# Kernel optimization log

Measured on AMD Instinct MI355X. Metric: run time of the kernel, lower is better.

Reference implementation:

```python
import jax, jax.numpy as jnp
import numpy as np

D_MODEL = 1024
N_HEADS = 16
D_K = D_MODEL // N_HEADS  # 64
SCALE = 1.0 / np.sqrt(D_K).astype(np.float32)


def setup_inputs() -> dict:
    key = jax.random.key(0)
    kx, kq, kk, kv, ko = jax.random.split(key, 5)
    B, S = 2, 2048
    s = 0.02  # keep pre-softmax logits in a sane range
    return {
        "x": jax.random.normal(kx, (B, S, D_MODEL), dtype=jnp.float32),
        "Wq": jax.random.normal(kq, (D_MODEL, D_MODEL), dtype=jnp.float32) * s,
        "Wk": jax.random.normal(kk, (D_MODEL, D_MODEL), dtype=jnp.float32) * s,
        "Wv": jax.random.normal(kv, (D_MODEL, D_MODEL), dtype=jnp.float32) * s,
        "Wo": jax.random.normal(ko, (D_MODEL, D_MODEL), dtype=jnp.float32) * s,
    }


def reference(x, Wq, Wk, Wv, Wo):
    # x: [B, S, D]; nn.Linear(bias=False) computes x @ W.T
    B, S, D = x.shape
    H, dk = N_HEADS, D_K

    def proj(W):
        # [B, S, D] -> [B, H, S, dk]
        return (x @ W.T).reshape(B, S, H, dk).transpose(0, 2, 1, 3)

    q = proj(Wq)
    k = proj(Wk)
    v = proj(Wv)

    # Flash tiling with online softmax is exact full attention (no mask):
    scores = jnp.einsum("bhqd,bhkd->bhqk", q, k) * SCALE  # [B,H,S,S]
    p = jax.nn.softmax(scores, axis=-1)
    o = jnp.einsum("bhqk,bhkd->bhqd", p, v)               # [B,H,S,dk]

    o = o.transpose(0, 2, 1, 3).reshape(B, S, D)
    return o @ Wo.T
```

## Files before the change

### kernel.cpp

```cpp
#include <hip/hip_runtime.h>
#include <cstdint>

typedef __attribute__((ext_vector_type(8))) __bf16 bf16x8;
typedef __attribute__((ext_vector_type(4))) float f32x4;
using u16 = unsigned short;
using u32 = unsigned int;

#define D_MODEL 1024
#define N_HEADS 16
#define D_K     64
#define SEQ     2048
#define BATCH   2
#define NTOKENS (BATCH * SEQ)
#define SCALE   0.125f
#define LOG2E   1.44269504088896340736f
#define C2      (SCALE * LOG2E)

__device__ __forceinline__ u16 f32_to_bf16(float f) {
    union { float f; u32 u; } v; v.f = f;
    u32 r = (v.u + 0x7fffu + ((v.u >> 16) & 1u)) >> 16;
    return (u16)r;
}

__device__ __forceinline__ u32 cvt_pk_bf16(float a, float b) {
    u32 r;
    asm("v_cvt_pk_bf16_f32 %0, %1, %2" : "=v"(r) : "v"(a), "v"(b));
    return r;
}

typedef const __attribute__((address_space(1))) u32* gas_ptr;
typedef __attribute__((address_space(3))) u32* las_ptr;
__device__ __forceinline__ void gl2lds16(const u16* g, u16* l) {
    __builtin_amdgcn_global_load_lds((gas_ptr)g, (las_ptr)l, 16, 0, 0);
}

__global__ __launch_bounds__(256) void cvt_all(const float* __restrict__ x,
                                               const float* __restrict__ Wq, const float* __restrict__ Wk,
                                               const float* __restrict__ Wv, const float* __restrict__ Wo,
                                               u16* __restrict__ xb,
                                               u16* __restrict__ wq, u16* __restrict__ wk,
                                               u16* __restrict__ wv, u16* __restrict__ wo) {
    const int NX = NTOKENS * D_MODEL;
    size_t i = (size_t)(blockIdx.x * 256 + threadIdx.x) * 4;
    const float* src; u16* dst; size_t off;
    if (i < (size_t)NX) { src = x; dst = xb; off = i; }
    else {
        size_t j = i - NX;
        int w = (int)(j >> 20);
        off = j & ((1u << 20) - 1);
        src = (w == 0) ? Wq : (w == 1) ? Wk : (w == 2) ? Wv : Wo;
        dst = (w == 0) ? wq : (w == 1) ? wk : (w == 2) ? wv : wo;
    }
    float4 f = *(const float4*)(src + off);
    u32 lo = (u32)f32_to_bf16(f.x) | ((u32)f32_to_bf16(f.y) << 16);
    u32 hi = (u32)f32_to_bf16(f.z) | ((u32)f32_to_bf16(f.w) << 16);
    uint2 o; o.x = lo; o.y = hi;
    *(uint2*)(dst + off) = o;
}

__global__ __launch_bounds__(256) void gemm_qkv(const u16* __restrict__ xb,
                                                const u16* __restrict__ wq,
                                                const u16* __restrict__ wk,
                                                const u16* __restrict__ wv,
                                                u16* __restrict__ Qb, u16* __restrict__ Kb,
                                                u16* __restrict__ Vt) {
    __shared__ __align__(16) u16 As[2][128 * 32];
    __shared__ __align__(16) u16 Bs[2][128 * 32];

    const int tid  = threadIdx.x;
    const int wave = tid >> 6, lane = tid & 63;
    const int quad = lane >> 4, l4 = lane & 15;
    const int wm = wave >> 1, wn = wave & 1;
    const int f = blockIdx.x;

    const u16 *Abase, *Bbase;
    if (f < 512) {
        const int m0 = (f & 31) * 128, t = f >> 5;
        Abase = xb + (size_t)m0 * D_MODEL;
        Bbase = ((t < 8) ? wq : wk) + (size_t)(t & 7) * 128 * D_MODEL;
    } else {
        const int g = f - 512;
        Abase = wv + (size_t)(g & 7) * 128 * D_MODEL;
        Bbase = xb + (size_t)(g >> 3) * 128 * D_MODEL;
    }

    f32x4 acc[4][4] = {};

    const int r0 = wave * 16 + (lane >> 2);
    const int ch = (lane & 3) * 8;
    const u16* Ag0 = Abase + (size_t)r0 * D_MODEL + ch;
    const u16* Bg0 = Bbase + (size_t)r0 * D_MODEL + ch;
    u16* AsW0 = As[0] + wave * 512;
    u16* AsW1 = As[1] + wave * 512;
    u16* BsW0 = Bs[0] + wave * 512;
    u16* BsW1 = Bs[1] + wave * 512;

    for (int kt = 0; kt < 16; ++kt) {
        const int ko = kt * 64;
        __syncthreads();
        gl2lds16(Ag0 + ko, AsW0);
        gl2lds16(Ag0 + (size_t)64 * D_MODEL + ko, AsW0 + 2048);
        gl2lds16(Bg0 + ko, BsW0);
        gl2lds16(Bg0 + (size_t)64 * D_MODEL + ko, BsW0 + 2048);
        gl2lds16(Ag0 + ko + 32, AsW1);
        gl2lds16(Ag0 + (size_t)64 * D_MODEL + ko + 32, AsW1 + 2048);
        gl2lds16(Bg0 + ko + 32, BsW1);
        gl2lds16(Bg0 + (size_t)64 * D_MODEL + ko + 32, BsW1 + 2048);
        __syncthreads();

#pragma unroll
        for (int s = 0; s < 2; ++s) {
            bf16x8 af[4], bfr[4];
#pragma unroll
            for (int mt = 0; mt < 4; mt++)
                af[mt] = *(const bf16x8*)&As[s][(wm * 64 + mt * 16 + l4) * 32 + quad * 8];
#pragma unroll
            for (int nt = 0; nt < 4; nt++)
                bfr[nt] = *(const bf16x8*)&Bs[s][(wn * 64 + nt * 16 + l4) * 32 + quad * 8];
#pragma unroll
            for (int mt = 0; mt < 4; mt++)
#pragma unroll
                for (int nt = 0; nt < 4; nt++)
                    acc[mt][nt] = __builtin_amdgcn_mfma_f32_16x16x32_bf16(af[mt], bfr[nt], acc[mt][nt], 0, 0, 0);
        }
    }

#pragma unroll
    for (int mt = 0; mt < 4; mt++)
#pragma unroll
        for (int nt = 0; nt < 4; nt++)
#pragma unroll
            for (int r = 0; r < 4; r++) {
                int mrow = wm * 64 + mt * 16 + quad * 4 + r;
                int ncol = wn * 64 + nt * 16 + l4;
                float v = acc[mt][nt][r];
                if (f < 512) {
                    const int m0 = (f & 31) * 128, t = f >> 5;
                    if (t < 8)
                        Qb[(size_t)(m0 + mrow) * D_MODEL + (t & 7) * 128 + ncol] = f32_to_bf16(v * C2);
                    else
                        Kb[(size_t)(m0 + mrow) * D_MODEL + (t & 7) * 128 + ncol] = f32_to_bf16(v);
                } else {
                    const int g = f - 512;
                    Vt[(size_t)((g & 7) * 128 + mrow) * NTOKENS + (g >> 3) * 128 + ncol] = f32_to_bf16(v);
                }
            }
}

__global__ __launch_bounds__(256) void gemm_out(const u16* __restrict__ A,
                                                const u16* __restrict__ Bw,
                                                float* __restrict__ C) {
    __shared__ __align__(16) u16 As[2][128 * 32];
    __shared__ __align__(16) u16 Bs[2][128 * 32];

    const int tid  = threadIdx.x;
    const int wave = tid >> 6, lane = tid & 63;
    const int quad = lane >> 4, l4 = lane & 15;
    const int wm = wave >> 1, wn = wave & 1;
    const int m0 = (blockIdx.x & 31) * 128, n0 = (blockIdx.x >> 5) * 128;

    f32x4 acc[4][4] = {};

    const int r0 = wave * 16 + (lane >> 2);
    const int ch = (lane & 3) * 8;
    const u16* Ag0 = A  + (size_t)(m0 + r0) * D_MODEL + ch;
    const u16* Bg0 = Bw + (size_t)(n0 + r0) * D_MODEL + ch;
    u16* AsW0 = As[0] + wave * 512;
    u16* AsW1 = As[1] + wave * 512;
    u16* BsW0 = Bs[0] + wave * 512;
    u16* BsW1 = Bs[1] + wave * 512;

    for (int kt = 0; kt < 16; ++kt) {
        const int ko = kt * 64;
        __syncthreads();
        gl2lds16(Ag0 + ko, AsW0);
        gl2lds16(Ag0 + (size_t)64 * D_MODEL + ko, AsW0 + 2048);
        gl2lds16(Bg0 + ko, BsW0);
        gl2lds16(Bg0 + (size_t)64 * D_MODEL + ko, BsW0 + 2048);
        gl2lds16(Ag0 + ko + 32, AsW1);
        gl2lds16(Ag0 + (size_t)64 * D_MODEL + ko + 32, AsW1 + 2048);
        gl2lds16(Bg0 + ko + 32, BsW1);
        gl2lds16(Bg0 + (size_t)64 * D_MODEL + ko + 32, BsW1 + 2048);
        __syncthreads();

#pragma unroll
        for (int s = 0; s < 2; ++s) {
            bf16x8 af[4], bfr[4];
#pragma unroll
            for (int mt = 0; mt < 4; mt++)
                af[mt] = *(const bf16x8*)&As[s][(wm * 64 + mt * 16 + l4) * 32 + quad * 8];
#pragma unroll
            for (int nt = 0; nt < 4; nt++)
                bfr[nt] = *(const bf16x8*)&Bs[s][(wn * 64 + nt * 16 + l4) * 32 + quad * 8];
#pragma unroll
            for (int mt = 0; mt < 4; mt++)
#pragma unroll
                for (int nt = 0; nt < 4; nt++)
                    acc[mt][nt] = __builtin_amdgcn_mfma_f32_16x16x32_bf16(af[mt], bfr[nt], acc[mt][nt], 0, 0, 0);
        }
    }

#pragma unroll
    for (int mt = 0; mt < 4; mt++)
#pragma unroll
        for (int nt = 0; nt < 4; nt++)
#pragma unroll
            for (int r = 0; r < 4; r++) {
                int mrow = wm * 64 + mt * 16 + quad * 4 + r;
                int ncol = wn * 64 + nt * 16 + l4;
                C[(size_t)(m0 + mrow) * D_MODEL + n0 + ncol] = acc[mt][nt][r];
            }
}

__global__ __launch_bounds__(512, 4) void attn(const u16* __restrict__ Q,
                                               const u16* __restrict__ K,
                                               const u16* __restrict__ Vt,
                                               u16* __restrict__ O) {
    __shared__ __align__(16) u16 smem[17664];
    u16* KsB = smem;
    u16* VsB = smem + 8192;
    const int KBUF = 4096, VBUF = 4096;

    const int tid  = threadIdx.x;
    const int wave = tid >> 6, lane = tid & 63;
    const int quad = lane >> 4, l4 = lane & 15;
    const int qg = wave & 3, kv = wave >> 2;
    const int bid = blockIdx.x;
    const int h  = (bid & 7) | (((bid >> 3) & 1) << 3);
    const int b  = (bid >> 4) & 1;
    const int q0 = (bid >> 5) * 128;
    const size_t headoff = (size_t)b * SEQ * D_MODEL + (size_t)h * D_K;

    const int sarr = tid >> 8;
    const int st   = tid & 255;
    const int srow = st >> 2, sc = st & 3;
    const int r7   = srow & 7;
    const u16* gsrc = (sarr == 0)
        ? K  + headoff + (size_t)srow * D_MODEL + sc * 16
        : Vt + (size_t)(h * 64 + srow) * NTOKENS + (size_t)b * SEQ + sc * 16;
    const size_t gstep = (sarr == 0) ? (size_t)64 * D_MODEL : 64;

    const int kd0 = srow * 64 + (((2 * sc)     ^ r7) * 8);
    const int kd1 = srow * 64 + (((2 * sc + 1) ^ r7) * 8);
    const int g32 = sc >> 1, vc = sc & 1;
    const int vw0 = srow * 64 + (((g32 * 4 + 0) ^ r7) * 8) + 4 * vc;
    const int vw1 = srow * 64 + (((g32 * 4 + 1) ^ r7) * 8) + 4 * vc;
    const int vw2 = srow * 64 + (((g32 * 4 + 2) ^ r7) * 8) + 4 * vc;
    const int vw3 = srow * 64 + (((g32 * 4 + 3) ^ r7) * 8) + 4 * vc;

    bf16x8 qa[2][2];
#pragma unroll
    for (int qs = 0; qs < 2; qs++) {
        const u16* qp = Q + headoff + (size_t)(q0 + qg * 32 + qs * 16 + l4) * D_MODEL + quad * 8;
        qa[qs][0] = *(const bf16x8*)qp;
        qa[qs][1] = *(const bf16x8*)(qp + 32);
    }

    union { u32 u[4]; bf16x8 v; } onesu;
#pragma unroll
    for (int i = 0; i < 4; i++) onesu.u[i] = 0x3F803F80u;

    int4 pr0 = *(const int4*)gsrc;
    int4 pr1 = *(const int4*)(gsrc + 8);

    f32x4 acc_o[2][4] = {};
    f32x4 acc_l[2] = {};

    const int sw7 = l4 & 7;

    for (int it = 0; it < 32; ++it) {
        if (sarr == 0) {
            u16* d = KsB + (it & 1) * KBUF;
            *(int4*)(d + kd0) = pr0;
            *(int4*)(d + kd1) = pr1;
        } else {
            u16* d = VsB + (it & 1) * VBUF;
            const uint2* h0 = (const uint2*)&pr0;
            const uint2* h1 = (const uint2*)&pr1;
            *(uint2*)(d + vw0) = h0[0];
            *(uint2*)(d + vw1) = h0[1];
            *(uint2*)(d + vw2) = h1[0];
            *(uint2*)(d + vw3) = h1[1];
        }
        __syncthreads();

        const u16* gn = gsrc + (size_t)((it + 1) & 31) * gstep;
        pr0 = *(const int4*)gn;
        pr1 = *(const int4*)(gn + 8);

        const u16* ksr = KsB + (it & 1) * KBUF;
        const u16* vsr = VsB + (it & 1) * VBUF;

        bf16x8 kb[2][2];
#pragma unroll
        for (int n2 = 0; n2 < 2; n2++) {
            const int krow = kv * 32 + n2 * 16 + l4;
            kb[n2][0] = *(const bf16x8*)&ksr[krow * 64 + ((quad       ^ sw7) * 8)];
            kb[n2][1] = *(const bf16x8*)&ksr[krow * 64 + (((4 + quad) ^ sw7) * 8)];
        }
        f32x4 sacc[2][2] = {};
        __builtin_amdgcn_s_setprio(1);
#pragma unroll
        for (int qs = 0; qs < 2; qs++)
#pragma unroll
            for (int n2 = 0; n2 < 2; n2++) {
                sacc[qs][n2] = __builtin_amdgcn_mfma_f32_16x16x32_bf16(kb[n2][0], qa[qs][0], sacc[qs][n2], 0, 0, 0);
                sacc[qs][n2] = __builtin_amdgcn_mfma_f32_16x16x32_bf16(kb[n2][1], qa[qs][1], sacc[qs][n2], 0, 0, 0);
            }
        __builtin_amdgcn_s_setprio(0);

        union { u32 u[4]; bf16x8 v; } pp[2];
#pragma unroll
        for (int qs = 0; qs < 2; qs++)
#pragma unroll
            for (int n2 = 0; n2 < 2; n2++) {
                float p0 = __builtin_amdgcn_exp2f(sacc[qs][n2][0]);
                float p1 = __builtin_amdgcn_exp2f(sacc[qs][n2][1]);
                float p2 = __builtin_amdgcn_exp2f(sacc[qs][n2][2]);
                float p3 = __builtin_amdgcn_exp2f(sacc[qs][n2][3]);
                pp[qs].u[n2 * 2]     = cvt_pk_bf16(p0, p1);
                pp[qs].u[n2 * 2 + 1] = cvt_pk_bf16(p2, p3);
            }

        __builtin_amdgcn_s_setprio(1);
#pragma unroll
        for (int dvt = 0; dvt < 4; dvt++) {
            const int vrow = dvt * 16 + l4;
            bf16x8 vfr = *(const bf16x8*)&vsr[vrow * 64 + ((((kv << 2) + quad) ^ sw7) * 8)];
#pragma unroll
            for (int qs = 0; qs < 2; qs++)
                acc_o[qs][dvt] = __builtin_amdgcn_mfma_f32_16x16x32_bf16(pp[qs].v, vfr, acc_o[qs][dvt], 0, 0, 0);
        }
#pragma unroll
        for (int qs = 0; qs < 2; qs++)
            acc_l[qs] = __builtin_amdgcn_mfma_f32_16x16x32_bf16(pp[qs].v, onesu.v, acc_l[qs], 0, 0, 0);
        __builtin_amdgcn_s_setprio(0);
    }

    const int OFS = 68;
    float* Of = (float*)smem;
    float* Lf = Of + 128 * OFS;
    __syncthreads();
    if (kv == 1) {
#pragma unroll
        for (int qs = 0; qs < 2; qs++) {
#pragma unroll
            for (int dvt = 0; dvt < 4; dvt++)
#pragma unroll
                for (int r = 0; r < 4; r++)
                    Of[(qg * 32 + qs * 16 + quad * 4 + r) * OFS + dvt * 16 + l4] = acc_o[qs][dvt][r];
            if (l4 == 0)
#pragma unroll
                for (int r = 0; r < 4; r++)
                    Lf[qg * 32 + qs * 16 + quad * 4 + r] = acc_l[qs][r];
        }
    }
    __syncthreads();
    if (kv == 0) {
#pragma unroll
        for (int qs = 0; qs < 2; qs++)
#pragma unroll
            for (int r = 0; r < 4; r++) {
                const int qi = qg * 32 + qs * 16 + quad * 4 + r;
                float ltot = acc_l[qs][r] + Lf[qi];
                float linv = 1.f / ltot;
                const int qrow = q0 + qi;
#pragma unroll
                for (int dvt = 0; dvt < 4; dvt++) {
                    float v = acc_o[qs][dvt][r] + Of[qi * OFS + dvt * 16 + l4];
                    O[headoff + (size_t)qrow * D_MODEL + dvt * 16 + l4] = f32_to_bf16(v * linv);
                }
            }
    }
}

extern "C" void kernel_launch(void* const* d_in, const int* in_sizes, int n_in,
                              void* d_out, int out_size, void* d_ws, size_t ws_size,
                              hipStream_t stream) {
    const float* x  = (const float*)d_in[0];
    const float* Wq = (const float*)d_in[1];
    const float* Wk = (const float*)d_in[2];
    const float* Wv = (const float*)d_in[3];
    const float* Wo = (const float*)d_in[4];

    const int NW = D_MODEL * D_MODEL;

    char* ws = (char*)d_ws;
    u16* xb = (u16*)ws;
    u16* wq = (u16*)(ws + (8u << 20));
    u16* wk = wq + NW;
    u16* wv = wk + NW;
    u16* wo = wv + NW;
    u16* Qb  = (u16*)(ws + (16u << 20));
    u16* Kb  = (u16*)(ws + (24u << 20));
    u16* Vtb = (u16*)(ws + (32u << 20));

    cvt_all<<<8192, 256, 0, stream>>>(x, Wq, Wk, Wv, Wo, xb, wq, wk, wv, wo);

    gemm_qkv<<<768, 256, 0, stream>>>(xb, wq, wk, wv, Qb, Kb, Vtb);

    attn<<<512, 512, 0, stream>>>(Qb, Kb, Vtb, xb);

    gemm_out<<<256, 256, 0, stream>>>(xb, wo, (float*)d_out);
}
```

Before: 183.4 us.

## Restructure GEMM core with prefetch pipelining and pre-swizzled global layout

```diff
diff --git a/kernel.cpp b/kernel.cpp
--- a/kernel.cpp
+++ b/kernel.cpp
@@ -55,159 +55,143 @@
     u32 lo = (u32)f32_to_bf16(f.x) | ((u32)f32_to_bf16(f.y) << 16);
     u32 hi = (u32)f32_to_bf16(f.z) | ((u32)f32_to_bf16(f.w) << 16);
     uint2 o; o.x = lo; o.y = hi;
-    *(uint2*)(dst + off) = o;
-}
-
-__global__ __launch_bounds__(256) void gemm_qkv(const u16* __restrict__ xb,
-                                                const u16* __restrict__ wq,
-                                                const u16* __restrict__ wk,
-                                                const u16* __restrict__ wv,
-                                                u16* __restrict__ Qb, u16* __restrict__ Kb,
-                                                u16* __restrict__ Vt) {
-    __shared__ __align__(16) u16 As[2][128 * 32];
-    __shared__ __align__(16) u16 Bs[2][128 * 32];
-
+    size_t osw = (off & ~(size_t)63) | ((((off >> 3) & 7) ^ ((off >> 10) & 7)) << 3) | (off & 7);
+    *(uint2*)(dst + osw) = o;
+}
+
+__device__ __forceinline__ void gemm_core_128(const u16* __restrict__ Ab,
+                                              const u16* __restrict__ Bb,
+                                              u16* __restrict__ sm,
+                                              f32x4 acc[4][4]) {
     const int tid  = threadIdx.x;
     const int wave = tid >> 6, lane = tid & 63;
-    const int quad = lane >> 4, l4 = lane & 15;
+    const int quad = lane >> 4, l4 = lane & 15, s7 = l4 & 7;
     const int wm = wave >> 1, wn = wave & 1;
-    const int f = blockIdx.x;
-
-    const u16 *Abase, *Bbase;
-    if (f < 512) {
-        const int m0 = (f & 31) * 128, t = f >> 5;
-        Abase = xb + (size_t)m0 * D_MODEL;
-        Bbase = ((t < 8) ? wq : wk) + (size_t)(t & 7) * 128 * D_MODEL;
+
+    const int srow = tid >> 3, sch = tid & 7;
+    const u16* Asrc = Ab + (size_t)srow * D_MODEL + sch * 8;
+    const u16* Bsrc = Bb + (size_t)srow * D_MODEL + sch * 8;
+
+#define STG8(base_, kt_) do {                                                         \
+    const size_t ko_ = (size_t)(kt_) * 64;                                            \
+    u16* const Ad_ = sm + (base_) + wave * 512;                                       \
+    u16* const Bd_ = sm + (base_) + 8192 + wave * 512;                                \
+    _Pragma("unroll")                                                                 \
+    for (int c_ = 0; c_ < 4; c_++)                                                    \
+        gl2lds16(Asrc + (size_t)c_ * 32 * D_MODEL + ko_, Ad_ + c_ * 2048);            \
+    _Pragma("unroll")                                                                 \
+    for (int c_ = 0; c_ < 4; c_++)                                                    \
+        gl2lds16(Bsrc + (size_t)c_ * 32 * D_MODEL + ko_, Bd_ + c_ * 2048);            \
+} while (0)
+
+    STG8(0, 0);
+    asm volatile("s_waitcnt vmcnt(0)" ::: "memory");
+    __builtin_amdgcn_s_barrier();
+
+    for (int kt = 0; kt < 16; ++kt) {
+        const int cur = (kt & 1) << 14;
+        if (kt < 15) {
+            if (kt & 1) STG8(0, kt + 1); else STG8(16384, kt + 1);
+        }
+        const u16* Ar = sm + cur;
+        const u16* Br = sm + cur + 8192;
+        bf16x8 af[4][2], bfr[4][2];
+#pragma unroll
+        for (int mt = 0; mt < 4; mt++) {
+            const int row = wm * 64 + mt * 16 + l4;
+#pragma unroll
+            for (int kk = 0; kk < 2; kk++)
+                af[mt][kk] = *(const bf16x8*)&Ar[row * 64 + (((kk << 2) + quad) ^ s7) * 8];
+        }
+#pragma unroll
+        for (int nt = 0; nt < 4; nt++) {
+            const int row = wn * 64 + nt * 16 + l4;
+#pragma unroll
+            for (int kk = 0; kk < 2; kk++)
+                bfr[nt][kk] = *(const bf16x8*)&Br[row * 64 + (((kk << 2) + quad) ^ s7) * 8];
+        }
+        __builtin_amdgcn_s_setprio(1);
+#pragma unroll
+        for (int kk = 0; kk < 2; kk++)
+#pragma unroll
+            for (int mt = 0; mt < 4; mt++)
+#pragma unroll
+                for (int nt = 0; nt < 4; nt++)
+                    acc[mt][nt] = __builtin_amdgcn_mfma_f32_16x16x32_bf16(af[mt][kk], bfr[nt][kk], acc[mt][nt], 0, 0, 0);
+        __builtin_amdgcn_s_setprio(0);
+        asm volatile("s_waitcnt vmcnt(0)" ::: "memory");
+        __builtin_amdgcn_s_barrier();
+    }
+#undef STG8
+}
+
+__global__ __launch_bounds__(256, 2) void gemm_qkv(const u16* __restrict__ xb,
+                                                   const u16* __restrict__ wq,
+                                                   const u16* __restrict__ wk,
+                                                   const u16* __restrict__ wv,
+                                                   u16* __restrict__ Qb, u16* __restrict__ Kb,
+                                                   u16* __restrict__ Vt) {
+    __shared__ __align__(16) u16 sm[32768];
+    const int bid = blockIdx.x;
+    const u16 *Ab, *Bb;
+    int m0, n0, sel;
+    if (bid < 512) {
+        sel = bid >> 8;
+        const int t = bid & 255;
+        m0 = (t >> 3) * 128; n0 = (t & 7) * 128;
+        Ab = xb + (size_t)m0 * D_MODEL;
+        Bb = (sel ? wk : wq) + (size_t)n0 * D_MODEL;
     } else {
-        const int g = f - 512;
-        Abase = wv + (size_t)(g & 7) * 128 * D_MODEL;
-        Bbase = xb + (size_t)(g >> 3) * 128 * D_MODEL;
+        sel = 2;
+        const int t = bid - 512;
+        m0 = (t >> 5) * 128; n0 = (t & 31) * 128;
+        Ab = wv + (size_t)m0 * D_MODEL;
+        Bb = xb + (size_t)n0 * D_MODEL;
     }
 
     f32x4 acc[4][4] = {};
-
-    const int r0 = wave * 16 + (lane >> 2);
-    const int ch = (lane & 3) * 8;
-    const u16* Ag0 = Abase + (size_t)r0 * D_MODEL + ch;
-    const u16* Bg0 = Bbase + (size_t)r0 * D_MODEL + ch;
-    u16* AsW0 = As[0] + wave * 512;
-    u16* AsW1 = As[1] + wave * 512;
-    u16* BsW0 = Bs[0] + wave * 512;
-    u16* BsW1 = Bs[1] + wave * 512;
-
-    for (int kt = 0; kt < 16; ++kt) {
-        const int ko = kt * 64;
-        __syncthreads();
-        gl2lds16(Ag0 + ko, AsW0);
-        gl2lds16(Ag0 + (size_t)64 * D_MODEL + ko, AsW0 + 2048);
-        gl2lds16(Bg0 + ko, BsW0);
-        gl2lds16(Bg0 + (size_t)64 * D_MODEL + ko, BsW0 + 2048);
-        gl2lds16(Ag0 + ko + 32, AsW1);
-        gl2lds16(Ag0 + (size_t)64 * D_MODEL + ko + 32, AsW1 + 2048);
-        gl2lds16(Bg0 + ko + 32, BsW1);
-        gl2lds16(Bg0 + (size_t)64 * D_MODEL + ko + 32, BsW1 + 2048);
-        __syncthreads();
-
-#pragma unroll
-        for (int s = 0; s < 2; ++s) {
-            bf16x8 af[4], bfr[4];
-#pragma unroll
-            for (int mt = 0; mt < 4; mt++)
-                af[mt] = *(const bf16x8*)&As[s][(wm * 64 + mt * 16 + l4) * 32 + quad * 8];
-#pragma unroll
-            for (int nt = 0; nt < 4; nt++)
-                bfr[nt] = *(const bf16x8*)&Bs[s][(wn * 64 + nt * 16 + l4) * 32 + quad * 8];
-#pragma unroll
-            for (int mt = 0; mt < 4; mt++)
-#pragma unroll
-                for (int nt = 0; nt < 4; nt++)
-                    acc[mt][nt] = __builtin_amdgcn_mfma_f32_16x16x32_bf16(af[mt], bfr[nt], acc[mt][nt], 0, 0, 0);
-        }
-    }
-
+    gemm_core_128(Ab, Bb, sm, acc);
+
+    const int lane = threadIdx.x & 63, quad = lane >> 4, l4 = lane & 15;
+    const int wave = threadIdx.x >> 6, wm = wave >> 1, wn = wave & 1;
 #pragma unroll
     for (int mt = 0; mt < 4; mt++)
 #pragma unroll
         for (int nt = 0; nt < 4; nt++)
 #pragma unroll
             for (int r = 0; r < 4; r++) {
-                int mrow = wm * 64 + mt * 16 + quad * 4 + r;
-                int ncol = wn * 64 + nt * 16 + l4;
-                float v = acc[mt][nt][r];
-                if (f < 512) {
-                    const int m0 = (f & 31) * 128, t = f >> 5;
-                    if (t < 8)
-                        Qb[(size_t)(m0 + mrow) * D_MODEL + (t & 7) * 128 + ncol] = f32_to_bf16(v * C2);
-                    else
-                        Kb[(size_t)(m0 + mrow) * D_MODEL + (t & 7) * 128 + ncol] = f32_to_bf16(v);
-                } else {
-                    const int g = f - 512;
-                    Vt[(size_t)((g & 7) * 128 + mrow) * NTOKENS + (g >> 3) * 128 + ncol] = f32_to_bf16(v);
-                }
-            }
-}
-
-__global__ __launch_bounds__(256) void gemm_out(const u16* __restrict__ A,
-                                                const u16* __restrict__ Bw,
-                                                float* __restrict__ C) {
-    __shared__ __align__(16) u16 As[2][128 * 32];
-    __shared__ __align__(16) u16 Bs[2][128 * 32];
-
-    const int tid  = threadIdx.x;
-    const int wave = tid >> 6, lane = tid & 63;
-    const int quad = lane >> 4, l4 = lane & 15;
-    const int wm = wave >> 1, wn = wave & 1;
-    const int m0 = (blockIdx.x & 31) * 128, n0 = (blockIdx.x >> 5) * 128;
+                const int mrow = wm * 64 + mt * 16 + quad * 4 + r;
+                const int ncol = wn * 64 + nt * 16 + l4;
+                const float v = acc[mt][nt][r];
+                if (sel == 0)
+                    Qb[(size_t)(m0 + mrow) * D_MODEL + n0 + ncol] = f32_to_bf16(v * C2);
+                else if (sel == 1)
+                    Kb[(size_t)(m0 + mrow) * D_MODEL + n0 + ncol] = f32_to_bf16(v);
+                else
+                    Vt[(size_t)(m0 + mrow) * NTOKENS + n0 + ncol] = f32_to_bf16(v);
+            }
+}
+
+__global__ __launch_bounds__(256, 2) void gemm_out(const u16* __restrict__ A,
+                                                   const u16* __restrict__ Bw,
+                                                   float* __restrict__ C) {
+    __shared__ __align__(16) u16 sm[32768];
+    const int bid = blockIdx.x;
+    const int m0 = (bid >> 3) * 128, n0 = (bid & 7) * 128;
 
     f32x4 acc[4][4] = {};
-
-    const int r0 = wave * 16 + (lane >> 2);
-    const int ch = (lane & 3) * 8;
-    const u16* Ag0 = A  + (size_t)(m0 + r0) * D_MODEL + ch;
-    const u16* Bg0 = Bw + (size_t)(n0 + r0) * D_MODEL + ch;
-    u16* AsW0 = As[0] + wave * 512;
-    u16* AsW1 = As[1] + wave * 512;
-    u16* BsW0 = Bs[0] + wave * 512;
-    u16* BsW1 = Bs[1] + wave * 512;
-
-    for (int kt = 0; kt < 16; ++kt) {
-        const int ko = kt * 64;
-        __syncthreads();
-        gl2lds16(Ag0 + ko, AsW0);
-        gl2lds16(Ag0 + (size_t)64 * D_MODEL + ko, AsW0 + 2048);
-        gl2lds16(Bg0 + ko, BsW0);
-        gl2lds16(Bg0 + (size_t)64 * D_MODEL + ko, BsW0 + 2048);
-        gl2lds16(Ag0 + ko + 32, AsW1);
-        gl2lds16(Ag0 + (size_t)64 * D_MODEL + ko + 32, AsW1 + 2048);
-        gl2lds16(Bg0 + ko + 32, BsW1);
-        gl2lds16(Bg0 + (size_t)64 * D_MODEL + ko + 32, BsW1 + 2048);
-        __syncthreads();
-
-#pragma unroll
-        for (int s = 0; s < 2; ++s) {
-            bf16x8 af[4], bfr[4];
-#pragma unroll
-            for (int mt = 0; mt < 4; mt++)
-                af[mt] = *(const bf16x8*)&As[s][(wm * 64 + mt * 16 + l4) * 32 + quad * 8];
-#pragma unroll
-            for (int nt = 0; nt < 4; nt++)
-                bfr[nt] = *(const bf16x8*)&Bs[s][(wn * 64 + nt * 16 + l4) * 32 + quad * 8];
-#pragma unroll
-            for (int mt = 0; mt < 4; mt++)
-#pragma unroll
-                for (int nt = 0; nt < 4; nt++)
-                    acc[mt][nt] = __builtin_amdgcn_mfma_f32_16x16x32_bf16(af[mt], bfr[nt], acc[mt][nt], 0, 0, 0);
-        }
-    }
-
+    gemm_core_128(A + (size_t)m0 * D_MODEL, Bw + (size_t)n0 * D_MODEL, sm, acc);
+
+    const int lane = threadIdx.x & 63, quad = lane >> 4, l4 = lane & 15;
+    const int wave = threadIdx.x >> 6, wm = wave >> 1, wn = wave & 1;
 #pragma unroll
     for (int mt = 0; mt < 4; mt++)
 #pragma unroll
         for (int nt = 0; nt < 4; nt++)
 #pragma unroll
             for (int r = 0; r < 4; r++) {
-                int mrow = wm * 64 + mt * 16 + quad * 4 + r;
-                int ncol = wn * 64 + nt * 16 + l4;
+                const int mrow = wm * 64 + mt * 16 + quad * 4 + r;
+                const int ncol = wn * 64 + nt * 16 + l4;
                 C[(size_t)(m0 + mrow) * D_MODEL + n0 + ncol] = acc[mt][nt][r];
             }
 }
@@ -368,7 +352,8 @@
 #pragma unroll
                 for (int dvt = 0; dvt < 4; dvt++) {
                     float v = acc_o[qs][dvt][r] + Of[qi * OFS + dvt * 16 + l4];
-                    O[headoff + (size_t)qrow * D_MODEL + dvt * 16 + l4] = f32_to_bf16(v * linv);
+                    const int csw = (((dvt * 2 + (l4 >> 3)) ^ (qrow & 7)) << 3) | (l4 & 7);
+                    O[headoff + (size_t)qrow * D_MODEL + csw] = f32_to_bf16(v * linv);
                 }
             }
     }
```

Result: faster. 178.9 us (-2.4%).
